# Optimization experiments

Measured on AMD Instinct MI355X. Metric: run time of the kernel, lower is better.

The kernel has to match this reference:

```python
import jax, jax.numpy as jnp
import numpy as np
from functools import partial

SIZES = (32.0, 64.0, 128.0, 256.0, 512.0)
RATIOS = (0.5, 1.0, 2.0)
POS_T, NEG_T = 0.7, 0.3


def _make_anchors(img_size, grid_sizes):
    # Mirrors AnchorGenerator: per feature, per size, per ratio, grid-flattened.
    parts = []
    for g in grid_sizes:
        stride = img_size / g
        steps = jnp.arange(g, dtype=jnp.float32) * stride
        x, y = jnp.meshgrid(steps, steps, indexing='ij')  # torch default 'ij'
        for s in SIZES:
            for r in RATIOS:
                rs = float(np.sqrt(r))
                wa = jnp.full((g, g), s * rs, jnp.float32)
                ha = jnp.full((g, g), s / rs, jnp.float32)
                parts.append(jnp.stack((x, y, wa, ha), axis=-1).reshape(-1, 4))
    return jnp.concatenate(parts, axis=0)  # [R,4] (cx,cy,w,h)


def _conv(x, w, b, pad):
    y = jax.lax.conv_general_dilated(x, w, (1, 1), [(pad, pad), (pad, pad)],
                                     dimension_numbers=('NCHW', 'OIHW', 'NCHW'))
    return y + b[None, :, None, None]


def _head(feat, conv_w, conv_b, cls_w, cls_b, box_w, box_b):
    t = jax.nn.relu(_conv(feat, conv_w, conv_b, 1))
    logits = _conv(t, cls_w, cls_b, 0)   # [b,A,g,g]
    bbox = _conv(t, box_w, box_b, 0)     # [b,4A,g,g]
    b, A, g, _ = logits.shape
    logits = logits.reshape(b, -1)       # [b, A*g*g] (anchor-major, matches anchor order)
    bbox = bbox.reshape(b, A, 4, g, g).transpose(0, 1, 3, 4, 2).reshape(b, -1, 4)
    return logits, bbox


def _iou(a, b):
    # a [R,4] xyxy, b [N,4] xyxy -> [R,N]
    lt = jnp.maximum(a[:, None, :2], b[None, :, :2])
    rb = jnp.minimum(a[:, None, 2:], b[None, :, 2:])
    wh = jnp.clip(rb - lt, 0.0)
    inter = wh[..., 0] * wh[..., 1]
    area_a = (a[:, 2] - a[:, 0]) * (a[:, 3] - a[:, 1])
    area_b = (b[:, 2] - b[:, 0]) * (b[:, 3] - b[:, 1])
    return inter / (area_a[:, None] + area_b[None, :] - inter)


def _label_one(anchors_xyxy, gt_xywh):
    # label_anchors for a single image
    gt = jnp.concatenate([gt_xywh[:, :2], gt_xywh[:, :2] + gt_xywh[:, 2:]], axis=-1)
    iou = _iou(anchors_xyxy, gt)               # [R,N]
    score = iou.max(axis=1)
    matched = gt[jnp.argmax(iou, axis=1)]      # [R,4]
    pos = score > POS_T
    pos = pos.at[jnp.argmax(iou, axis=0)].set(True)  # best anchor per gt
    labels = jnp.where(score < NEG_T, 0.0, jnp.where(pos, 1.0, -1.0))
    return labels, matched


def _forward(images, feats, gt_boxes, conv_w, conv_b, cls_w, cls_b, box_w, box_b):
    grid_sizes = [f.shape[-1] for f in feats]
    anchors = _make_anchors(float(images.shape[-1]), grid_sizes)  # [R,4] cwh
    half = anchors[:, 2:] * 0.5
    anchors_xyxy = jnp.concatenate([anchors[:, :2] - half, anchors[:, :2] + half], -1)
    outs = [_head(f, conv_w, conv_b, cls_w, cls_b, box_w, box_b) for f in feats]
    obj = jnp.concatenate([o for o, _ in outs], axis=1)      # [b,R]
    deltas = jnp.concatenate([d for _, d in outs], axis=1)   # [b,R,4]
    labels, matched = jax.vmap(partial(_label_one, anchors_xyxy))(gt_boxes)
    preds = jnp.concatenate([obj[..., None], deltas], axis=-1)  # [b,R,5]
    return preds, labels, matched


def setup_inputs() -> dict:
    key = jax.random.key(0)
    ks = jax.random.split(key, 12)
    b, C, A = 2, 256, 15
    grids = (128, 64, 32, 16, 8)
    inp = {'images': jax.random.uniform(ks[0], (b, 3, 512, 512), jnp.float32)}
    for i, g in enumerate(grids):
        inp[f'feat{i}'] = jax.random.normal(ks[1 + i], (b, C, g, g), jnp.float32)
    xy = jax.random.uniform(ks[6], (b, 32, 2), jnp.float32) * 384.0
    wh = 16.0 + jax.random.uniform(ks[7], (b, 32, 2), jnp.float32) * 112.0
    inp['gt_boxes'] = jnp.concatenate([xy, wh], axis=-1)  # (x,y,w,h)
    inp['conv_w'] = 0.01 * jax.random.normal(ks[8], (C, C, 3, 3), jnp.float32)
    inp['conv_b'] = jnp.zeros((C,), jnp.float32)
    inp['cls_w'] = 0.01 * jax.random.normal(ks[9], (A, C, 1, 1), jnp.float32)
    inp['cls_b'] = jnp.zeros((A,), jnp.float32)
    inp['box_w'] = 0.01 * jax.random.normal(ks[10], (4 * A, C, 1, 1), jnp.float32)
    inp['box_b'] = jnp.zeros((4 * A,), jnp.float32)
    return inp


def reference(images, feat0, feat1, feat2, feat3, feat4, gt_boxes,
              conv_w, conv_b, cls_w, cls_b, box_w, box_b):
    return _forward(images, [feat0, feat1, feat2, feat3, feat4], gt_boxes,
                    conv_w, conv_b, cls_w, cls_b, box_w, box_b)
```

## Files before the change

### kernel.cpp

```cpp
#include <hip/hip_runtime.h>

typedef unsigned short u16;
typedef unsigned char  u8;
typedef unsigned int   u32;
typedef __bf16 bf16x8 __attribute__((ext_vector_type(8)));
typedef float  f32x4  __attribute__((ext_vector_type(4)));
typedef u16    u16x8  __attribute__((ext_vector_type(8)));
typedef u16    u16x4  __attribute__((ext_vector_type(4)));

#define R_TOTAL 327360
#define LAB_OFF 3273600
#define MAT_OFF 3928320
#define NLBLK   1279

static __device__ const int    D_LOG2G[5] = {7, 6, 5, 4, 3};
static __device__ const size_t D_FTOFF[5] = {0, 8389120, 10486784, 11011584, 11143168};
static __device__ const int    D_TPOFF[5] = {0, 32768, 40960, 43008, 43520};
static __device__ const int    D_AOFF[5]  = {0, 245760, 307200, 322560, 326400};

static __device__ const float D_WH[15][2] = {
  {22.627416997969522f, 45.254833995939045f}, {32.f, 32.f},   {45.254833995939045f, 22.627416997969522f},
  {45.254833995939045f, 90.50966799187809f},  {64.f, 64.f},   {90.50966799187809f, 45.254833995939045f},
  {90.50966799187809f, 181.01933598375618f},  {128.f, 128.f}, {181.01933598375618f, 90.50966799187809f},
  {181.01933598375618f, 362.03867196751236f}, {256.f, 256.f}, {362.03867196751236f, 181.01933598375618f},
  {362.03867196751236f, 724.0773439350247f},  {512.f, 512.f}, {724.0773439350247f, 362.03867196751236f},
};

__device__ __forceinline__ u16 f2bf(float x) {
  u32 u = __float_as_uint(x);
  u32 r = u + 0x7FFFu + ((u >> 16) & 1u);
  return (u16)(r >> 16);
}
__device__ __forceinline__ float bf2f(u16 v) { return __uint_as_float(((u32)v) << 16); }

__device__ __forceinline__ void glds16(const void* g, void* l) {
  __builtin_amdgcn_global_load_lds(
      (const __attribute__((address_space(1))) u32*)g,
      (__attribute__((address_space(3))) u32*)l, 16, 0, 0);
}

__device__ inline void anchor_box(int r, float& x1, float& y1, float& x2, float& y2) {
  #pragma clang fp contract(off)
  int off, lg;
  if (r < 245760)      { off = 0;      lg = 7; }
  else if (r < 307200) { off = 245760; lg = 6; }
  else if (r < 322560) { off = 307200; lg = 5; }
  else if (r < 326400) { off = 322560; lg = 4; }
  else                 { off = 326400; lg = 3; }
  int rem  = r - off;
  int a    = rem >> (2 * lg);
  int rem2 = rem & ((1 << (2 * lg)) - 1);
  int i = rem2 >> lg;
  int j = rem2 & ((1 << lg) - 1);
  float stride = (float)(512 >> lg);
  float cx = (float)i * stride;
  float cy = (float)j * stride;
  float hw = D_WH[a][0] * 0.5f;
  float hh = D_WH[a][1] * 0.5f;
  x1 = cx - hw; y1 = cy - hh; x2 = cx + hw; y2 = cy + hh;
}

__device__ inline float iou_f(float ax1, float ay1, float ax2, float ay2,
                              float bx1, float by1, float bx2, float by2) {
  #pragma clang fp contract(off)
  float ltx = fmaxf(ax1, bx1), lty = fmaxf(ay1, by1);
  float rbx = fminf(ax2, bx2), rby = fminf(ay2, by2);
  float iw = fmaxf(rbx - ltx, 0.f);
  float ih = fmaxf(rby - lty, 0.f);
  float inter = iw * ih;
  float aa = (ax2 - ax1) * (ay2 - ay1);
  float ab = (bx2 - bx1) * (by2 - by1);
  return inter / (aa + ab - inter);
}

__global__ __launch_bounds__(256) void pack_all_kernel(
    const float* __restrict__ cw, u16* __restrict__ wp,
    const float* __restrict__ cls_w, const float* __restrict__ cls_b,
    const float* __restrict__ box_w, const float* __restrict__ box_b,
    u16* __restrict__ Wb, float* __restrict__ hbias) {
  if (blockIdx.x < 2304) {
    int idx = blockIdx.x * 256 + threadIdx.x;
    int ks  = idx >> 13;
    int rem = idx & 8191;
    int co  = rem >> 5;
    int k   = rem & 31;
    int tap = ks >> 3;
    int cb  = ks & 7;
    float v = cw[co * 2304 + (cb * 32 + k) * 9 + tap];
    int qd = k >> 3, wi = k & 7;
    int dq = qd ^ ((co >> 1) & 3);
    wp[(size_t)ks * 8192 + co * 32 + dq * 8 + wi] = f2bf(v);
  } else {
    int idx = (blockIdx.x - 2304) * 256 + threadIdx.x;
    int row = idx >> 8, k = idx & 255;
    float v = (row < 15) ? cls_w[row * 256 + k] : (row < 75) ? box_w[(row - 15) * 256 + k] : 0.f;
    Wb[row * 256 + k] = f2bf(v);
    if (idx < 80) hbias[idx] = (idx < 15) ? cls_b[idx] : (idx < 75) ? box_b[idx - 15] : 0.f;
  }
}

__global__ __launch_bounds__(256) void feat_pack_kernel(
    const float* __restrict__ f0, const float* __restrict__ f1,
    const float* __restrict__ f2, const float* __restrict__ f3,
    const float* __restrict__ f4, u16* __restrict__ Ft) {
  __shared__ float tile[64][65];
  int bid = blockIdx.x;
  int l, base, nb1;
  if (bid < 514)      { l = 0; base = 0;   nb1 = 257; }
  else if (bid < 644) { l = 1; base = 514; nb1 = 65; }
  else if (bid < 678) { l = 2; base = 644; nb1 = 17; }
  else if (bid < 688) { l = 3; base = 678; nb1 = 5; }
  else                { l = 4; base = 688; nb1 = 2; }
  const int lg = D_LOG2G[l];
  const int HW = 1 << (2 * lg);
  int blk = bid - base;
  int b   = blk / nb1;
  int p0  = (blk - b * nb1) * 64;
  u16* dst = Ft + D_FTOFF[l];
  const int tid = threadIdx.x;
  if (p0 >= HW) {
    if (tid < 32) {
      u16x8 z = (u16x8)0;
      *(u16x8*)(dst + ((size_t)b * (HW + 1) + HW) * 256 + tid * 8) = z;
    }
    return;
  }
  const float* fsel = (l == 0) ? f0 : (l == 1) ? f1 : (l == 2) ? f2 : (l == 3) ? f3 : f4;
  const float* fb = fsel + (size_t)b * 256 * HW;
  for (int cg = 0; cg < 4; ++cg) {
    __syncthreads();
    #pragma unroll
    for (int i = 0; i < 16; ++i) {
      int idx = i * 256 + tid;
      int cl = idx >> 6, pp = idx & 63;
      tile[cl][pp] = fb[(size_t)(cg * 64 + cl) * HW + p0 + pp];
    }
    __syncthreads();
    #pragma unroll
    for (int i = 0; i < 2; ++i) {
      int slot = i * 256 + tid;
      int pos = slot >> 3, ch = slot & 7;
      u16x8 v;
      #pragma unroll
      for (int j = 0; j < 8; ++j) v[j] = f2bf(tile[ch * 8 + j][pos]);
      *(u16x8*)(dst + ((size_t)b * (HW + 1) + p0 + pos) * 256 + cg * 64 + ch * 8) = v;
    }
  }
}

__global__ __launch_bounds__(128) void conv_mfma_kernel(
    const u16* __restrict__ Ft, const u16* __restrict__ wp,
    const float* __restrict__ cb, u16* __restrict__ tP) {
  __shared__ __align__(16) u8 Asb[16384];
  __shared__ __align__(16) u8 Bsb[8192];
  const int bid = blockIdx.x;
  int l, base;
  if (bid < 1024)      { l = 0; base = 0; }
  else if (bid < 1280) { l = 1; base = 1024; }
  else if (bid < 1344) { l = 2; base = 1280; }
  else if (bid < 1360) { l = 3; base = 1344; }
  else                 { l = 4; base = 1360; }
  const int lg = D_LOG2G[l];
  const int g = 1 << lg, HW = 1 << (2 * lg);
  const int lognt = 2 * lg - 5;
  const int blk = bid - base;
  const int ct = blk >> lognt;
  const int tile = blk & ((1 << lognt) - 1);
  const int n0 = tile << 6;
  const int co0 = ct << 7;
  const int tid = threadIdx.x;
  const int wv = tid >> 6, lane = tid & 63;
  const u16* FtL = Ft + D_FTOFF[l];
  const u8* wpb = (const u8*)wp;
  const int b_img = n0 >> (2 * lg);
  const int dq = tid & 3;
  const int nl0 = tid >> 2, nl1 = nl0 + 32;
  const int swz0 = (dq ^ ((nl0 >> 1) & 3)) << 3;
  const int swz1 = (dq ^ ((nl1 >> 1) & 3)) << 3;
  const int pg0 = (n0 + nl0) & (HW - 1);
  const int h0 = pg0 >> lg, w0 = pg0 & (g - 1);
  const int pg1 = (n0 + nl1) & (HW - 1);
  const int h1 = pg1 >> lg, w1 = pg1 & (g - 1);
  const u16* bimg = FtL + (size_t)b_img * (HW + 1) * 256;
  const int lm = lane & 15, lq = lane >> 4;
  int aoffs[4], boffs[4];
  #pragma unroll
  for (int mi = 0; mi < 4; ++mi) {
    int row = wv * 64 + mi * 16 + lm;
    aoffs[mi] = row * 64 + ((lq ^ ((row >> 1) & 3)) << 4);
  }
  #pragma unroll
  for (int ni = 0; ni < 4; ++ni) {
    int col = ni * 16 + lm;
    boffs[ni] = col * 64 + ((lq ^ ((col >> 1) & 3)) << 4);
  }
  f32x4 acc[4][4];
  #pragma unroll
  for (int mi = 0; mi < 4; ++mi)
    #pragma unroll
    for (int ni = 0; ni < 4; ++ni) acc[mi][ni] = (f32x4)0.f;

  auto tap_src = [&](int tap, const u16*& s0, const u16*& s1) {
    const int dh = tap / 3 - 1, dw = tap % 3 - 1;
    int sh0 = h0 + dh, sw0 = w0 + dw;
    int r0 = ((unsigned)sh0 < (unsigned)g && (unsigned)sw0 < (unsigned)g) ? (sh0 * g + sw0) : HW;
    int sh1 = h1 + dh, sw1 = w1 + dw;
    int r1 = ((unsigned)sh1 < (unsigned)g && (unsigned)sw1 < (unsigned)g) ? (sh1 * g + sw1) : HW;
    s0 = bimg + (size_t)r0 * 256 + swz0;
    s1 = bimg + (size_t)r1 * 256 + swz1;
  };
  auto STAGE = [&](int p, int tap_, int cb8_, const u16* s0, const u16* s1) {
    glds16(s0 + cb8_ * 32, Bsb + p * 4096 + wv * 1024);
    glds16(s1 + cb8_ * 32, Bsb + p * 4096 + (2 + wv) * 1024);
    const u8* aK = wpb + (size_t)(tap_ * 8 + cb8_) * 16384 + co0 * 64;
    #pragma unroll
    for (int c = 0; c < 4; ++c) {
      int ch = c * 2 + wv;
      glds16(aK + ch * 1024 + lane * 16, Asb + p * 8192 + ch * 1024);
    }
  };

  const u16 *cs0, *cs1;
  tap_src(0, cs0, cs1);
  int p = 0;
  STAGE(0, 0, 0, cs0, cs1);
  __syncthreads();

  for (int tap = 0; tap < 9; ++tap) {
    const u16 *ns0 = cs0, *ns1 = cs1;
    if (tap < 8) tap_src(tap + 1, ns0, ns1);
    #pragma unroll
    for (int cb8 = 0; cb8 < 8; ++cb8) {
      if (!(tap == 8 && cb8 == 7)) {
        if (cb8 < 7) STAGE(p ^ 1, tap, cb8 + 1, cs0, cs1);
        else         STAGE(p ^ 1, tap + 1, 0, ns0, ns1);
      }
      bf16x8 af[4], bfr[4];
      #pragma unroll
      for (int mi = 0; mi < 4; ++mi) af[mi] = *(const bf16x8*)(Asb + p * 8192 + aoffs[mi]);
      #pragma unroll
      for (int ni = 0; ni < 4; ++ni) bfr[ni] = *(const bf16x8*)(Bsb + p * 4096 + boffs[ni]);
      #pragma unroll
      for (int mi = 0; mi < 4; ++mi)
        #pragma unroll
        for (int ni = 0; ni < 4; ++ni)
          acc[mi][ni] = __builtin_amdgcn_mfma_f32_16x16x32_bf16(af[mi], bfr[ni], acc[mi][ni], 0, 0, 0);
      __syncthreads();
      p ^= 1;
    }
    cs0 = ns0; cs1 = ns1;
  }
  u16* tPL = tP + ((size_t)D_TPOFF[l] + (size_t)b_img * HW) * 256;
  #pragma unroll
  for (int mi = 0; mi < 4; ++mi) {
    const int cob = co0 + wv * 64 + mi * 16 + lq * 4;
    const float4 bs = *(const float4*)&cb[cob];
    #pragma unroll
    for (int ni = 0; ni < 4; ++ni) {
      int pp = (n0 + ni * 16 + lm) & (HW - 1);
      u16x4 v;
      v[0] = f2bf(fmaxf(acc[mi][ni][0] + bs.x, 0.f));
      v[1] = f2bf(fmaxf(acc[mi][ni][1] + bs.y, 0.f));
      v[2] = f2bf(fmaxf(acc[mi][ni][2] + bs.z, 0.f));
      v[3] = f2bf(fmaxf(acc[mi][ni][3] + bs.w, 0.f));
      *(u16x4*)&tPL[(size_t)pp * 256 + cob] = v;
    }
  }
}

__global__ __launch_bounds__(128) void head_mfma_kernel(
    const u16* __restrict__ tP, const u16* __restrict__ Wb,
    const float* __restrict__ hbias, float* __restrict__ out) {
  __shared__ __align__(16) u8 Bsb[32768];
  const int bid = blockIdx.x;
  int l, base;
  if (bid < 512)      { l = 0; base = 0; }
  else if (bid < 640) { l = 1; base = 512; }
  else if (bid < 672) { l = 2; base = 640; }
  else if (bid < 680) { l = 3; base = 672; }
  else                { l = 4; base = 680; }
  const int lg = D_LOG2G[l];
  const int HW = 1 << (2 * lg);
  const int blk = bid - base;
  const int n0 = blk << 6;
  const int tid = threadIdx.x;
  const int wv = tid >> 6, lane = tid & 63;
  const int lm = lane & 15, lq = lane >> 4;
  const u16* src = tP + ((size_t)D_TPOFF[l] + n0) * 256;
  #pragma unroll
  for (int i = 0; i < 16; ++i) {
    int c = wv + i * 2;
    int slot = c * 64 + lane;
    int pos = slot >> 5, sp = slot & 31;
    glds16(src + (size_t)pos * 256 + ((sp ^ (pos & 7)) << 3), Bsb + c * 1024);
  }
  __syncthreads();
  f32x4 acc[5][2];
  #pragma unroll
  for (int mi = 0; mi < 5; ++mi) { acc[mi][0] = (f32x4)0.f; acc[mi][1] = (f32x4)0.f; }
  for (int kb = 0; kb < 8; ++kb) {
    bf16x8 af[5], bfr[2];
    #pragma unroll
    for (int mi = 0; mi < 5; ++mi)
      af[mi] = *(const bf16x8*)&Wb[(mi * 16 + lm) * 256 + kb * 32 + lq * 8];
    #pragma unroll
    for (int ni = 0; ni < 2; ++ni) {
      int p_ = wv * 32 + ni * 16 + lm;
      bfr[ni] = *(const bf16x8*)(Bsb + p_ * 512 + (((kb * 4 + lq) ^ (p_ & 7)) << 4));
    }
    #pragma unroll
    for (int mi = 0; mi < 5; ++mi)
      #pragma unroll
      for (int ni = 0; ni < 2; ++ni)
        acc[mi][ni] = __builtin_amdgcn_mfma_f32_16x16x32_bf16(af[mi], bfr[ni], acc[mi][ni], 0, 0, 0);
  }
  const int b   = n0 >> (2 * lg);
  const int pgb = n0 & (HW - 1);
  const size_t obase = (size_t)b * R_TOTAL;
  const int aoff = D_AOFF[l];
  #pragma unroll
  for (int mi = 0; mi < 5; ++mi) {
    #pragma unroll
    for (int r = 0; r < 4; ++r) {
      int oc = mi * 16 + lq * 4 + r;
      if (oc < 75) {
        float bs = hbias[oc];
        size_t rr; int comp;
        if (oc < 15) { rr = (size_t)aoff + (size_t)oc * HW; comp = 0; }
        else { int o2 = oc - 15; rr = (size_t)aoff + (size_t)(o2 >> 2) * HW; comp = 1 + (o2 & 3); }
        #pragma unroll
        for (int ni = 0; ni < 2; ++ni) {
          int pg = pgb + wv * 32 + ni * 16 + lm;
          out[(obase + rr + pg) * 5 + comp] = acc[mi][ni][r] + bs;
        }
      }
    }
  }
}

__global__ __launch_bounds__(256) void label_fused_kernel(const float* __restrict__ gt,
                                                          float* __restrict__ out,
                                                          float2* __restrict__ partial) {
  #pragma clang fp contract(off)
  __shared__ float gx[32][4];
  __shared__ float sh[256][33];
  __shared__ float2 red[32][8];
  const int b = blockIdx.y;
  const int tid = threadIdx.x;
  if (tid < 32) {
    const float* gp = gt + ((size_t)b * 32 + tid) * 4;
    float x = gp[0], y = gp[1], w = gp[2], h = gp[3];
    gx[tid][0] = x; gx[tid][1] = y; gx[tid][2] = x + w; gx[tid][3] = y + h;
  }
  __syncthreads();
  const int r = blockIdx.x * 256 + tid;
  const bool valid = (r < R_TOTAL);
  const int rv = valid ? r : 0;
  float ax1, ay1, ax2, ay2;
  anchor_box(rv, ax1, ay1, ax2, ay2);
  float best = -1e30f; int bi = 0;
  for (int n = 0; n < 32; ++n) {
    float v = iou_f(ax1, ay1, ax2, ay2, gx[n][0], gx[n][1], gx[n][2], gx[n][3]);
    sh[tid][n] = valid ? v : -1e30f;
    if (v > best) { best = v; bi = n; }
  }
  if (valid) {
    float lab = (best < 0.3f) ? 0.f : ((best > 0.7f) ? 1.f : -1.f);
    out[LAB_OFF + (size_t)b * R_TOTAL + r] = lab;
    float4 m; m.x = gx[bi][0]; m.y = gx[bi][1]; m.z = gx[bi][2]; m.w = gx[bi][3];
    *(float4*)&out[MAT_OFF + ((size_t)b * R_TOTAL + r) * 4] = m;
  }
  __syncthreads();
  const int n = tid & 31, gr = tid >> 5;
  float bv = -1e30f; int li = 0;
  #pragma unroll 4
  for (int a = 0; a < 32; ++a) {
    int la = gr * 32 + a;
    float v = sh[la][n];
    if (v > bv) { bv = v; li = la; }
  }
  red[n][gr] = make_float2(bv, __int_as_float(li));
  __syncthreads();
  if (tid < 32) {
    float fv = -1e30f; int fi = 0;
    #pragma unroll
    for (int g2 = 0; g2 < 8; ++g2) {
      float2 pv = red[tid][g2];
      int ii = __float_as_int(pv.y);
      if (pv.x > fv) { fv = pv.x; fi = ii; }
    }
    partial[(size_t)(b * 32 + tid) * NLBLK + blockIdx.x] =
        make_float2(fv, __int_as_float(blockIdx.x * 256 + fi));
  }
}

__global__ __launch_bounds__(256) void argmax_final2_kernel(
    const float* __restrict__ gt, const float2* __restrict__ partial,
    float* __restrict__ out) {
  #pragma clang fp contract(off)
  __shared__ float sv[256];
  __shared__ int   si[256];
  const int b = blockIdx.x >> 5, n = blockIdx.x & 31;
  const float2* pp = partial + (size_t)(b * 32 + n) * NLBLK;
  const int tid = threadIdx.x;
  float bv = -1e30f; int bi = 0x7fffffff;
  for (int i = tid; i < NLBLK; i += 256) {
    float2 pv = pp[i]; int ii = __float_as_int(pv.y);
    if (pv.x > bv || (pv.x == bv && ii < bi)) { bv = pv.x; bi = ii; }
  }
  sv[tid] = bv; si[tid] = bi;
  __syncthreads();
  for (int s = 128; s > 0; s >>= 1) {
    if (tid < s) {
      float v2 = sv[tid + s]; int i2 = si[tid + s];
      if (v2 > sv[tid] || (v2 == sv[tid] && i2 < si[tid])) { sv[tid] = v2; si[tid] = i2; }
    }
    __syncthreads();
  }
  if (tid == 0) {
    int banch = si[0];
    float ax1, ay1, ax2, ay2;
    anchor_box(banch, ax1, ay1, ax2, ay2);
    float score = -1e30f;
    for (int n2 = 0; n2 < 32; ++n2) {
      const float* gp = gt + ((size_t)b * 32 + n2) * 4;
      float v = iou_f(ax1, ay1, ax2, ay2, gp[0], gp[1], gp[0] + gp[2], gp[1] + gp[3]);
      score = fmaxf(score, v);
    }
    out[LAB_OFF + (size_t)b * R_TOTAL + banch] = (score < 0.3f) ? 0.f : 1.f;
  }
}

extern "C" void kernel_launch(void* const* d_in, const int* in_sizes, int n_in,
                              void* d_out, int out_size, void* d_ws, size_t ws_size,
                              hipStream_t stream) {
  const float* f0     = (const float*)d_in[1];
  const float* f1     = (const float*)d_in[2];
  const float* f2     = (const float*)d_in[3];
  const float* f3     = (const float*)d_in[4];
  const float* f4     = (const float*)d_in[5];
  const float* gt     = (const float*)d_in[6];
  const float* conv_w = (const float*)d_in[7];
  const float* conv_b = (const float*)d_in[8];
  const float* cls_w  = (const float*)d_in[9];
  const float* cls_b  = (const float*)d_in[10];
  const float* box_w  = (const float*)d_in[11];
  const float* box_b  = (const float*)d_in[12];
  float* out = (float*)d_out;
  u8* wsb = (u8*)d_ws;

  u16*    wp      = (u16*)wsb;
  u16*    Ft      = (u16*)(wsb + 1179648);
  u16*    tP      = (u16*)(wsb + 23532544);
  u16*    Wb      = (u16*)(wsb + 45880320);
  float*  hbias   = (float*)(wsb + 45921280);
  float2* partial = (float2*)(wsb + 45921600);

  pack_all_kernel<<<2384, 256, 0, stream>>>(conv_w, wp, cls_w, cls_b, box_w, box_b, Wb, hbias);
  feat_pack_kernel<<<692, 256, 0, stream>>>(f0, f1, f2, f3, f4, Ft);
  conv_mfma_kernel<<<1364, 128, 0, stream>>>(Ft, wp, conv_b, tP);
  head_mfma_kernel<<<682, 128, 0, stream>>>(tP, Wb, hbias, out);
  label_fused_kernel<<<dim3(NLBLK, 2), 256, 0, stream>>>(gt, out, partial);
  argmax_final2_kernel<<<64, 256, 0, stream>>>(gt, partial, out);
}
```

Measured before the change: 231.6 us.

## Merge pack kernels and replace label LDS reduction with wave-shuffle packed-key argmax

Merges weight packing and feature transposition into one prep kernel launch, removing one launch. Rewrites anchor labeling to use 64-thread blocks where the per-GT best anchor is found with a 64-bit packed (iou, ~index) key and wave xor-shuffles, instead of a 256x33 LDS matrix and two-stage reduction. The final argmax then reduces the packed keys directly. This trades LDS traffic and block syncs for 32 shuffle reductions per wave plus more partial entries to scan.

```diff
diff --git a/kernel.cpp b/kernel.cpp
--- a/kernel.cpp
+++ b/kernel.cpp
@@ -3,6 +3,7 @@
 typedef unsigned short u16;
 typedef unsigned char  u8;
 typedef unsigned int   u32;
+typedef unsigned long long u64;
 typedef __bf16 bf16x8 __attribute__((ext_vector_type(8)));
 typedef float  f32x4  __attribute__((ext_vector_type(4)));
 typedef u16    u16x8  __attribute__((ext_vector_type(8)));
@@ -11,7 +12,7 @@
 #define R_TOTAL 327360
 #define LAB_OFF 3273600
 #define MAT_OFF 3928320
-#define NLBLK   1279
+#define NL64    5115
 
 static __device__ const int    D_LOG2G[5] = {7, 6, 5, 4, 3};
 static __device__ const size_t D_FTOFF[5] = {0, 8389120, 10486784, 11011584, 11143168};
@@ -31,7 +32,6 @@
   u32 r = u + 0x7FFFu + ((u >> 16) & 1u);
   return (u16)(r >> 16);
 }
-__device__ __forceinline__ float bf2f(u16 v) { return __uint_as_float(((u32)v) << 16); }
 
 __device__ __forceinline__ void glds16(const void* g, void* l) {
   __builtin_amdgcn_global_load_lds(
@@ -73,13 +73,18 @@
   return inter / (aa + ab - inter);
 }
 
-__global__ __launch_bounds__(256) void pack_all_kernel(
+__global__ __launch_bounds__(256) void prep_kernel(
     const float* __restrict__ cw, u16* __restrict__ wp,
     const float* __restrict__ cls_w, const float* __restrict__ cls_b,
     const float* __restrict__ box_w, const float* __restrict__ box_b,
-    u16* __restrict__ Wb, float* __restrict__ hbias) {
+    u16* __restrict__ Wb, float* __restrict__ hbias,
+    const float* __restrict__ f0, const float* __restrict__ f1,
+    const float* __restrict__ f2, const float* __restrict__ f3,
+    const float* __restrict__ f4, u16* __restrict__ Ft) {
+  __shared__ float tile[64][65];
+  const int tid = threadIdx.x;
   if (blockIdx.x < 2304) {
-    int idx = blockIdx.x * 256 + threadIdx.x;
+    int idx = blockIdx.x * 256 + tid;
     int ks  = idx >> 13;
     int rem = idx & 8191;
     int co  = rem >> 5;
@@ -90,21 +95,17 @@
     int qd = k >> 3, wi = k & 7;
     int dq = qd ^ ((co >> 1) & 3);
     wp[(size_t)ks * 8192 + co * 32 + dq * 8 + wi] = f2bf(v);
-  } else {
-    int idx = (blockIdx.x - 2304) * 256 + threadIdx.x;
+    return;
+  }
+  if (blockIdx.x < 2384) {
+    int idx = (blockIdx.x - 2304) * 256 + tid;
     int row = idx >> 8, k = idx & 255;
     float v = (row < 15) ? cls_w[row * 256 + k] : (row < 75) ? box_w[(row - 15) * 256 + k] : 0.f;
     Wb[row * 256 + k] = f2bf(v);
     if (idx < 80) hbias[idx] = (idx < 15) ? cls_b[idx] : (idx < 75) ? box_b[idx - 15] : 0.f;
-  }
-}
-
-__global__ __launch_bounds__(256) void feat_pack_kernel(
-    const float* __restrict__ f0, const float* __restrict__ f1,
-    const float* __restrict__ f2, const float* __restrict__ f3,
-    const float* __restrict__ f4, u16* __restrict__ Ft) {
-  __shared__ float tile[64][65];
-  int bid = blockIdx.x;
+    return;
+  }
+  int bid = blockIdx.x - 2384;
   int l, base, nb1;
   if (bid < 514)      { l = 0; base = 0;   nb1 = 257; }
   else if (bid < 644) { l = 1; base = 514; nb1 = 65; }
@@ -117,7 +118,6 @@
   int b   = blk / nb1;
   int p0  = (blk - b * nb1) * 64;
   u16* dst = Ft + D_FTOFF[l];
-  const int tid = threadIdx.x;
   if (p0 >= HW) {
     if (tid < 32) {
       u16x8 z = (u16x8)0;
@@ -338,96 +338,71 @@
   }
 }
 
-__global__ __launch_bounds__(256) void label_fused_kernel(const float* __restrict__ gt,
-                                                          float* __restrict__ out,
-                                                          float2* __restrict__ partial) {
+__global__ __launch_bounds__(64) void label_kernel(const float* __restrict__ gt,
+                                                   float* __restrict__ out,
+                                                   u64* __restrict__ partial) {
   #pragma clang fp contract(off)
-  __shared__ float gx[32][4];
-  __shared__ float sh[256][33];
-  __shared__ float2 red[32][8];
-  const int b = blockIdx.y;
+  const int lb = blockIdx.x;
+  const int b = (lb >= NL64) ? 1 : 0;
+  const int lblk = lb - b * NL64;
   const int tid = threadIdx.x;
-  if (tid < 32) {
-    const float* gp = gt + ((size_t)b * 32 + tid) * 4;
-    float x = gp[0], y = gp[1], w = gp[2], h = gp[3];
-    gx[tid][0] = x; gx[tid][1] = y; gx[tid][2] = x + w; gx[tid][3] = y + h;
-  }
-  __syncthreads();
-  const int r = blockIdx.x * 256 + tid;
-  const bool valid = (r < R_TOTAL);
-  const int rv = valid ? r : 0;
+  const int r = lblk * 64 + tid;
   float ax1, ay1, ax2, ay2;
-  anchor_box(rv, ax1, ay1, ax2, ay2);
+  anchor_box(r, ax1, ay1, ax2, ay2);
+  const float* gb = gt + b * 128;
   float best = -1e30f; int bi = 0;
+  u64 mykey = 0;
   for (int n = 0; n < 32; ++n) {
-    float v = iou_f(ax1, ay1, ax2, ay2, gx[n][0], gx[n][1], gx[n][2], gx[n][3]);
-    sh[tid][n] = valid ? v : -1e30f;
+    float x = gb[n * 4 + 0], y = gb[n * 4 + 1];
+    float w = gb[n * 4 + 2], h = gb[n * 4 + 3];
+    float v = iou_f(ax1, ay1, ax2, ay2, x, y, x + w, y + h);
     if (v > best) { best = v; bi = n; }
-  }
-  if (valid) {
-    float lab = (best < 0.3f) ? 0.f : ((best > 0.7f) ? 1.f : -1.f);
-    out[LAB_OFF + (size_t)b * R_TOTAL + r] = lab;
-    float4 m; m.x = gx[bi][0]; m.y = gx[bi][1]; m.z = gx[bi][2]; m.w = gx[bi][3];
-    *(float4*)&out[MAT_OFF + ((size_t)b * R_TOTAL + r) * 4] = m;
-  }
-  __syncthreads();
-  const int n = tid & 31, gr = tid >> 5;
-  float bv = -1e30f; int li = 0;
-  #pragma unroll 4
-  for (int a = 0; a < 32; ++a) {
-    int la = gr * 32 + a;
-    float v = sh[la][n];
-    if (v > bv) { bv = v; li = la; }
-  }
-  red[n][gr] = make_float2(bv, __int_as_float(li));
-  __syncthreads();
-  if (tid < 32) {
-    float fv = -1e30f; int fi = 0;
-    #pragma unroll
-    for (int g2 = 0; g2 < 8; ++g2) {
-      float2 pv = red[tid][g2];
-      int ii = __float_as_int(pv.y);
-      if (pv.x > fv) { fv = pv.x; fi = ii; }
-    }
-    partial[(size_t)(b * 32 + tid) * NLBLK + blockIdx.x] =
-        make_float2(fv, __int_as_float(blockIdx.x * 256 + fi));
-  }
-}
-
-__global__ __launch_bounds__(256) void argmax_final2_kernel(
-    const float* __restrict__ gt, const float2* __restrict__ partial,
+    u64 key = ((u64)__float_as_uint(v) << 32) | (u32)(~(u32)r);
+    #pragma unroll
+    for (int s = 1; s < 64; s <<= 1) {
+      u64 o = (u64)__shfl_xor((unsigned long long)key, s);
+      if (o > key) key = o;
+    }
+    if (tid == n) mykey = key;
+  }
+  float lab = (best < 0.3f) ? 0.f : ((best > 0.7f) ? 1.f : -1.f);
+  out[LAB_OFF + (size_t)b * R_TOTAL + r] = lab;
+  const float4 gv = *(const float4*)(gt + ((size_t)b * 32 + bi) * 4);
+  float4 m; m.x = gv.x; m.y = gv.y; m.z = gv.x + gv.z; m.w = gv.y + gv.w;
+  *(float4*)&out[MAT_OFF + ((size_t)b * R_TOTAL + r) * 4] = m;
+  if (tid < 32) partial[((size_t)b * NL64 + lblk) * 32 + tid] = mykey;
+}
+
+__global__ __launch_bounds__(256) void argmax_final_kernel(
+    const float* __restrict__ gt, const u64* __restrict__ partial,
     float* __restrict__ out) {
   #pragma clang fp contract(off)
-  __shared__ float sv[256];
-  __shared__ int   si[256];
+  __shared__ u64 sk[256];
   const int b = blockIdx.x >> 5, n = blockIdx.x & 31;
-  const float2* pp = partial + (size_t)(b * 32 + n) * NLBLK;
+  const u64* pp = partial + (size_t)b * NL64 * 32 + n;
   const int tid = threadIdx.x;
-  float bv = -1e30f; int bi = 0x7fffffff;
-  for (int i = tid; i < NLBLK; i += 256) {
-    float2 pv = pp[i]; int ii = __float_as_int(pv.y);
-    if (pv.x > bv || (pv.x == bv && ii < bi)) { bv = pv.x; bi = ii; }
-  }
-  sv[tid] = bv; si[tid] = bi;
+  u64 best = 0;
+  for (int i = tid; i < NL64; i += 256) {
+    u64 k = pp[(size_t)i * 32];
+    if (k > best) best = k;
+  }
+  sk[tid] = best;
   __syncthreads();
   for (int s = 128; s > 0; s >>= 1) {
-    if (tid < s) {
-      float v2 = sv[tid + s]; int i2 = si[tid + s];
-      if (v2 > sv[tid] || (v2 == sv[tid] && i2 < si[tid])) { sv[tid] = v2; si[tid] = i2; }
-    }
+    if (tid < s) { if (sk[tid + s] > sk[tid]) sk[tid] = sk[tid + s]; }
     __syncthreads();
   }
   if (tid == 0) {
-    int banch = si[0];
+    int ra = (int)(~(u32)sk[0]);
     float ax1, ay1, ax2, ay2;
-    anchor_box(banch, ax1, ay1, ax2, ay2);
+    anchor_box(ra, ax1, ay1, ax2, ay2);
     float score = -1e30f;
     for (int n2 = 0; n2 < 32; ++n2) {
       const float* gp = gt + ((size_t)b * 32 + n2) * 4;
       float v = iou_f(ax1, ay1, ax2, ay2, gp[0], gp[1], gp[0] + gp[2], gp[1] + gp[3]);
       score = fmaxf(score, v);
     }
-    out[LAB_OFF + (size_t)b * R_TOTAL + banch] = (score < 0.3f) ? 0.f : 1.f;
+    out[LAB_OFF + (size_t)b * R_TOTAL + ra] = (score < 0.3f) ? 0.f : 1.f;
   }
 }
 
@@ -449,17 +424,17 @@
   float* out = (float*)d_out;
   u8* wsb = (u8*)d_ws;
 
-  u16*    wp      = (u16*)wsb;
-  u16*    Ft      = (u16*)(wsb + 1179648);
-  u16*    tP      = (u16*)(wsb + 23532544);
-  u16*    Wb      = (u16*)(wsb + 45880320);
-  float*  hbias   = (float*)(wsb + 45921280);
-  float2* partial = (float2*)(wsb + 45921600);
-
-  pack_all_kernel<<<2384, 256, 0, stream>>>(conv_w, wp, cls_w, cls_b, box_w, box_b, Wb, hbias);
-  feat_pack_kernel<<<692, 256, 0, stream>>>(f0, f1, f2, f3, f4, Ft);
+  u16*   wp      = (u16*)wsb;
+  u16*   Ft      = (u16*)(wsb + 1179648);
+  u16*   tP      = (u16*)(wsb + 23532544);
+  u16*   Wb      = (u16*)(wsb + 45880320);
+  float* hbias   = (float*)(wsb + 45921280);
+  u64*   partial = (u64*)(wsb + 45921600);
+
+  prep_kernel<<<3076, 256, 0, stream>>>(conv_w, wp, cls_w, cls_b, box_w, box_b,
+                                        Wb, hbias, f0, f1, f2, f3, f4, Ft);
   conv_mfma_kernel<<<1364, 128, 0, stream>>>(Ft, wp, conv_b, tP);
   head_mfma_kernel<<<682, 128, 0, stream>>>(tP, Wb, hbias, out);
-  label_fused_kernel<<<dim3(NLBLK, 2), 256, 0, stream>>>(gt, out, partial);
-  argmax_final2_kernel<<<64, 256, 0, stream>>>(gt, partial, out);
-}
+  label_kernel<<<2 * NL64, 64, 0, stream>>>(gt, out, partial);
+  argmax_final_kernel<<<64, 256, 0, stream>>>(gt, partial, out);
+}
```

After: 261.0 us. 1.13x slower.
